# Optimization experiments

Hardware: AMD Instinct MI355X
Metric: run time of the kernel (lower is better)

The kernel has to match this reference:

```python
import jax, jax.numpy as jnp
import numpy as np

BETA = 0.5  # exp-sum normalization exponent (not a true softmax)


def setup_inputs() -> dict:
    key = jax.random.key(0)
    ks = jax.random.split(key, 12)
    b, h = 1024, 200
    item_num, region_num, user_num = 50000, 1000, 10000
    d, hid = 128, 128  # embed_size == hidden_size (required by the bmm reshape)
    std = 0.01
    return {
        "history": jax.random.randint(ks[0], (1, b, h), 0, item_num),
        "target": jax.random.randint(ks[1], (1, b), 0, item_num),
        "history_region": jax.random.randint(ks[2], (1, b, h), 0, region_num),
        "target_region": jax.random.randint(ks[3], (1, b), 0, region_num),
        "history_visit_rate": jax.random.uniform(ks[4], (1, h), dtype=jnp.float32),
        "dist_mat": jax.random.uniform(ks[5], (b, h), dtype=jnp.float32),
        "uid": 7,
        "embed_target": std * jax.random.normal(ks[6], (item_num, d // 2), dtype=jnp.float32),
        "embed_region": std * jax.random.normal(ks[7], (region_num, d // 2), dtype=jnp.float32),
        "embed_dist": std * jax.random.normal(ks[8], (user_num, region_num), dtype=jnp.float32),
        "Wq": jax.random.normal(ks[9], (hid, d), dtype=jnp.float32) * (1.0 / np.sqrt(d)),
        "Wk": jax.random.normal(ks[10], (hid, d), dtype=jnp.float32) * (1.0 / np.sqrt(d)),
        "Wv": jax.random.normal(ks[11], (d, d), dtype=jnp.float32) * (1.0 / np.sqrt(d)),
    }


def reference(history, target, history_region, target_region, history_visit_rate,
              dist_mat, uid, embed_target, embed_region, embed_dist, Wq, Wk, Wv):
    h_idx = history[0]            # [b, h]
    tgt = target[0]               # [b]
    hr = history_region[0]        # [b, h]
    tr = target_region[0]         # [b]
    hv = history_visit_rate[0]    # [h]
    b, hlen = h_idx.shape

    # embedding gathers + concat (target half | region half)
    hist_emb = jnp.concatenate([embed_target[h_idx], embed_region[hr]], axis=-1)  # [b,h,d]
    tgt_emb = jnp.concatenate([embed_target[tgt], embed_region[tr]], axis=-1)     # [b,d]
    hd = embed_dist[uid][hr]      # [b, h]
    td = embed_dist[uid][tr]      # [b]
    d = tgt_emb.shape[1]

    # QKV projections (torch Linear: y = x @ W.T)
    q = tgt_emb @ Wq.T            # [b, d]  (hidden == d)
    k = hist_emb @ Wk.T           # [b, h, d]
    v = hist_emb @ Wv.T           # [b, h, d]

    # faithful to original: key reshaped (NOT transposed) to [b, d, h]
    k_r = k.reshape(b, d, hlen)
    scores = jnp.einsum('bd,bdh->bh', q, k_r) / jnp.sqrt(jnp.float32(d))  # [b,h]

    # exp / beta-normalized attention with equality mask
    mask = (h_idx != tgt[:, None]).astype(scores.dtype)
    exp_A = jnp.exp(scores) * mask                          # [b,h]
    exp_sum = jnp.sum(exp_A, axis=-1) ** BETA               # [b]
    attn = exp_A / exp_sum[:, None]                         # [b,h]

    # geo weights: td @ hd is a vector-matrix product -> [h], broadcast over b
    geo = jnp.exp(-1.0 / (jax.nn.relu(td @ hd) + 1.0) * dist_mat)  # [b,h]

    result1 = v * (attn + geo)[..., None]                   # [b,h,d]
    result2 = hist_emb * jnp.broadcast_to(hv, (b, hlen))[..., None]
    result = result1 + result2                              # [b,h,d]

    pred = jnp.einsum('bhd,bd->b', result, tgt_emb)         # bmm + sum over h
    return jax.nn.sigmoid(pred)
```

## Files before the change

### kernel.cpp

```cpp
#include <hip/hip_runtime.h>

typedef unsigned short USH;
typedef unsigned int   UIN;

static constexpr int Bn = 1024;
static constexpr int Hn = 200;
static constexpr int Dn = 128;
static constexpr int Dh = 64;
static constexpr int NITEM = 50000;
static constexpr int NREG  = 1000;
static constexpr int MT = 64;
static constexpr int AB_A_BLOCKS = (NITEM + MT - 1) / MT;
static constexpr int AB_B_BLOCKS = (NREG  + MT - 1) / MT;
static constexpr int AB_TOT = AB_A_BLOCKS + AB_B_BLOCKS;
static constexpr int QU_BLOCKS = Bn / 4;
static constexpr int WTS = 132;
static constexpr int ETS = 69;
static constexpr int CR  = 50;
static constexpr int AFS = 192;

__device__ __forceinline__ float bf2f(USH u) {
  return __uint_as_float(((UIN)u) << 16);
}
__device__ __forceinline__ float2 pb2f2(UIN p) {
  float2 r;
  r.x = __uint_as_float(p << 16);
  r.y = __uint_as_float(p & 0xffff0000u);
  return r;
}
__device__ __forceinline__ USH f2b(float f) {
  UIN x = __float_as_uint(f);
  return (USH)((x + 0x7fffu + ((x >> 16) & 1u)) >> 16);
}
__device__ __forceinline__ UIN addpk(UIN u, UIN v) {
  float2 a = pb2f2(u), b = pb2f2(v);
  return (UIN)f2b(a.x + b.x) | ((UIN)f2b(a.y + b.y) << 16);
}

__global__ __launch_bounds__(256) void g_kernel(
    const int* __restrict__ hregion, const int* __restrict__ tregion,
    const float* __restrict__ embed_dist, const int* __restrict__ uid,
    float* __restrict__ g) {
  int c = threadIdx.x;
  const float* row = embed_dist + (size_t)uid[0] * NREG;
  float acc = 0.f;
  int ibase = blockIdx.x * 16;
  for (int ii = 0; ii < 16; ii++) {
    int i = ibase + ii;
    float td = row[tregion[i]];
    if (c < Hn) acc += td * row[hregion[(size_t)i * Hn + c]];
  }
  if (c < Hn) atomicAdd(&g[c], acc);
}

__global__ __launch_bounds__(256, 2) void ab_kernel(
    const float* __restrict__ Et, const float* __restrict__ Er,
    const float* __restrict__ Wk, const float* __restrict__ Wq,
    const float* __restrict__ Wv, const int* __restrict__ target,
    const int* __restrict__ tregion,
    USH* __restrict__ Af, USH* __restrict__ Bf,
    float* __restrict__ qvt, float* __restrict__ uvt) {
  __shared__ float wt[64 * WTS];
  __shared__ float et[MT * ETS];
  int blk = blockIdx.x, tid = threadIdx.x;

  if (blk >= AB_TOT) {
    float* te = wt;
    int i0 = (blk - AB_TOT) * 4;
#pragma unroll
    for (int v = 0; v < 2; v++) {
      int idx = v * 256 + tid;
      int ii = idx >> 7, d = idx & 127;
      int it = i0 + ii;
      te[ii * 128 + d] = (d < 64) ? Et[(size_t)target[it] * Dh + d]
                                  : Er[(size_t)tregion[it] * Dh + (d - 64)];
    }
    __syncthreads();
    int j = tid & 127, half = tid >> 7;
    float a0 = 0.f, a1 = 0.f, a2 = 0.f, a3 = 0.f;
    if (half == 0) {
      const float* wr = Wq + (size_t)j * Dn;
#pragma unroll 8
      for (int k = 0; k < 128; k++) {
        float w = wr[k];
        a0 += w * te[k]; a1 += w * te[128 + k];
        a2 += w * te[256 + k]; a3 += w * te[384 + k];
      }
      const float s = 0.088388347648318447f;
      qvt[(size_t)(i0 + 0) * Dn + j] = a0 * s;
      qvt[(size_t)(i0 + 1) * Dn + j] = a1 * s;
      qvt[(size_t)(i0 + 2) * Dn + j] = a2 * s;
      qvt[(size_t)(i0 + 3) * Dn + j] = a3 * s;
    } else {
      int d = j;
#pragma unroll 8
      for (int k = 0; k < 128; k++) {
        float w = Wv[(size_t)k * Dn + d];
        a0 += w * te[k]; a1 += w * te[128 + k];
        a2 += w * te[256 + k]; a3 += w * te[384 + k];
      }
      uvt[(size_t)(i0 + 0) * Dn + d] = a0;
      uvt[(size_t)(i0 + 1) * Dn + d] = a1;
      uvt[(size_t)(i0 + 2) * Dn + d] = a2;
      uvt[(size_t)(i0 + 3) * Dn + d] = a3;
    }
    return;
  }

  const float* E; USH* Out; int nmax, base, koff;
  if (blk < AB_A_BLOCKS) { E = Et; Out = Af; nmax = NITEM; base = blk * MT; koff = 0; }
  else { E = Er; Out = Bf; nmax = NREG; base = (blk - AB_A_BLOCKS) * MT; koff = 64; }

#pragma unroll
  for (int p = 0; p < 8; p++) {
    int idx = p * 256 + tid;
    int row = idx >> 4, c4 = idx & 15;
    float4 w = *reinterpret_cast<const float4*>(Wk + (size_t)row * Dn + koff + c4 * 4);
    wt[(c4 * 4 + 0) * WTS + row] = w.x;
    wt[(c4 * 4 + 1) * WTS + row] = w.y;
    wt[(c4 * 4 + 2) * WTS + row] = w.z;
    wt[(c4 * 4 + 3) * WTS + row] = w.w;
  }
#pragma unroll
  for (int p = 0; p < 4; p++) {
    int idx = p * 256 + tid;
    int m = idx >> 4, c4 = idx & 15;
    int gi = base + m;
    float4 e = make_float4(0.f, 0.f, 0.f, 0.f);
    if (gi < nmax) e = *reinterpret_cast<const float4*>(E + (size_t)gi * Dh + c4 * 4);
    et[m * ETS + c4 * 4 + 0] = e.x;
    et[m * ETS + c4 * 4 + 1] = e.y;
    et[m * ETS + c4 * 4 + 2] = e.z;
    et[m * ETS + c4 * 4 + 3] = e.w;
  }
  __syncthreads();

#pragma unroll
  for (int q = 0; q < 8; q++) {
    int idx = q * 256 + tid;
    int m = idx >> 5, kp = idx & 31;
    int gi = base + m;
    if (gi < nmax) {
      UIN pk = (UIN)f2b(et[m * ETS + 2 * kp]) | ((UIN)f2b(et[m * ETS + 2 * kp + 1]) << 16);
      *reinterpret_cast<UIN*>(Out + (size_t)gi * AFS + 128 + 2 * kp) = pk;
    }
  }

  int jt = tid & 15, it = tid >> 4;
  const float* wb = wt + jt * 8;
  const float* eb = et + (it * 4) * ETS;
  float c[4][8];
#pragma unroll
  for (int ii = 0; ii < 4; ii++)
#pragma unroll
    for (int jj = 0; jj < 8; jj++) c[ii][jj] = 0.f;

#pragma unroll 2
  for (int k = 0; k < 64; k++) {
    float4 w0 = *reinterpret_cast<const float4*>(wb + (size_t)k * WTS);
    float4 w1 = *reinterpret_cast<const float4*>(wb + (size_t)k * WTS + 4);
    float e0 = eb[k], e1 = eb[ETS + k], e2 = eb[2 * ETS + k], e3 = eb[3 * ETS + k];
    c[0][0] += e0 * w0.x; c[0][1] += e0 * w0.y; c[0][2] += e0 * w0.z; c[0][3] += e0 * w0.w;
    c[0][4] += e0 * w1.x; c[0][5] += e0 * w1.y; c[0][6] += e0 * w1.z; c[0][7] += e0 * w1.w;
    c[1][0] += e1 * w0.x; c[1][1] += e1 * w0.y; c[1][2] += e1 * w0.z; c[1][3] += e1 * w0.w;
    c[1][4] += e1 * w1.x; c[1][5] += e1 * w1.y; c[1][6] += e1 * w1.z; c[1][7] += e1 * w1.w;
    c[2][0] += e2 * w0.x; c[2][1] += e2 * w0.y; c[2][2] += e2 * w0.z; c[2][3] += e2 * w0.w;
    c[2][4] += e2 * w1.x; c[2][5] += e2 * w1.y; c[2][6] += e2 * w1.z; c[2][7] += e2 * w1.w;
    c[3][0] += e3 * w0.x; c[3][1] += e3 * w0.y; c[3][2] += e3 * w0.z; c[3][3] += e3 * w0.w;
    c[3][4] += e3 * w1.x; c[3][5] += e3 * w1.y; c[3][6] += e3 * w1.z; c[3][7] += e3 * w1.w;
  }

#pragma unroll
  for (int ii = 0; ii < 4; ii++) {
    int item = base + it * 4 + ii;
    if (item < nmax) {
      uint4 pk;
      pk.x = (UIN)f2b(c[ii][0]) | ((UIN)f2b(c[ii][1]) << 16);
      pk.y = (UIN)f2b(c[ii][2]) | ((UIN)f2b(c[ii][3]) << 16);
      pk.z = (UIN)f2b(c[ii][4]) | ((UIN)f2b(c[ii][5]) << 16);
      pk.w = (UIN)f2b(c[ii][6]) | ((UIN)f2b(c[ii][7]) << 16);
      *reinterpret_cast<uint4*>(Out + (size_t)item * AFS + jt * 8) = pk;
    }
  }
}

__global__ __launch_bounds__(256, 4) void sc_kernel(
    const int* __restrict__ history, const int* __restrict__ target,
    const int* __restrict__ hregion, const int* __restrict__ tregion,
    const float* __restrict__ Et, const float* __restrict__ Er,
    const float* __restrict__ qvt, const float* __restrict__ uvt,
    const USH* __restrict__ Af, const USH* __restrict__ Bf,
    float* __restrict__ psc, float2* __restrict__ s12) {
  __shared__ USH kvs[CR * Dn];
  __shared__ float tgtE[128], uvf[128], qv[32];
  int b = blockIdx.x, i = b >> 2, h = b & 3;
  int tid = threadIdx.x;
  const int* hrow = history + (size_t)i * Hn + CR * h;
  const int* rrow = hregion + (size_t)i * Hn + CR * h;

  if (tid < 128) {
    tgtE[tid] = (tid < 64) ? Et[(size_t)target[i] * Dh + tid]
                           : Er[(size_t)tregion[i] * Dh + (tid - 64)];
  } else {
    uvf[tid - 128] = uvt[(size_t)i * Dn + (tid - 128)];
  }
  if (tid < 32) qv[tid] = qvt[(size_t)i * Dn + 32 * h + tid];

  {
    int rlane = tid & 15, rgrp = tid >> 4;
#pragma unroll
    for (int p = 0; p < 4; p++) {
      int t = p * 16 + rgrp;
      if (t < CR) {
        int ia = hrow[t], ib = rrow[t];
        uint4 av = *reinterpret_cast<const uint4*>(Af + (size_t)ia * AFS + rlane * 8);
        uint4 bv = *reinterpret_cast<const uint4*>(Bf + (size_t)ib * AFS + rlane * 8);
        uint4 pk;
        pk.x = addpk(av.x, bv.x); pk.y = addpk(av.y, bv.y);
        pk.z = addpk(av.z, bv.z); pk.w = addpk(av.w, bv.w);
        *reinterpret_cast<uint4*>(&kvs[t * Dn + rlane * 8]) = pk;
      }
    }
  }
  __syncthreads();

  {
    int l8 = tid & 7, r8 = tid >> 3;
#pragma unroll
    for (int p = 0; p < 2; p++) {
      int t = p * 32 + r8;
      if (t < CR) {
        int ia = hrow[t], ib = rrow[t];
        uint4 e = *reinterpret_cast<const uint4*>(Af + (size_t)ia * AFS + 128 + l8 * 8);
        uint4 r = *reinterpret_cast<const uint4*>(Bf + (size_t)ib * AFS + 128 + l8 * 8);
        float2 e0 = pb2f2(e.x), e1 = pb2f2(e.y), e2 = pb2f2(e.z), e3 = pb2f2(e.w);
        float2 r0 = pb2f2(r.x), r1 = pb2f2(r.y), r2 = pb2f2(r.z), r3 = pb2f2(r.w);
        const float* u0 = &uvf[l8 * 8];       const float* t0 = &tgtE[l8 * 8];
        const float* u1 = &uvf[64 + l8 * 8];  const float* t1 = &tgtE[64 + l8 * 8];
        float s1a = e0.x * u0[0] + e0.y * u0[1] + e1.x * u0[2] + e1.y * u0[3]
                  + e2.x * u0[4] + e2.y * u0[5] + e3.x * u0[6] + e3.y * u0[7]
                  + r0.x * u1[0] + r0.y * u1[1] + r1.x * u1[2] + r1.y * u1[3]
                  + r2.x * u1[4] + r2.y * u1[5] + r3.x * u1[6] + r3.y * u1[7];
        float s2a = e0.x * t0[0] + e0.y * t0[1] + e1.x * t0[2] + e1.y * t0[3]
                  + e2.x * t0[4] + e2.y * t0[5] + e3.x * t0[6] + e3.y * t0[7]
                  + r0.x * t1[0] + r0.y * t1[1] + r1.x * t1[2] + r1.y * t1[3]
                  + r2.x * t1[4] + r2.y * t1[5] + r3.x * t1[6] + r3.y * t1[7];
        s1a += __shfl_xor(s1a, 1, 64); s2a += __shfl_xor(s2a, 1, 64);
        s1a += __shfl_xor(s1a, 2, 64); s2a += __shfl_xor(s2a, 2, 64);
        s1a += __shfl_xor(s1a, 4, 64); s2a += __shfl_xor(s2a, 4, 64);
        if (l8 == 0) s12[(size_t)i * Hn + CR * h + t] = make_float2(s1a, s2a);
      }
    }
  }

  if (tid < Hn) {
    float acc = 0.f;
    const USH* kp = &kvs[tid];
#pragma unroll
    for (int a = 0; a < 32; a++) acc += qv[a] * bf2f(kp[a * 200]);
    psc[((size_t)i * 4 + h) * Hn + tid] = acc;
  }
}

__global__ __launch_bounds__(256, 8) void ep_kernel(
    const int* __restrict__ history, const int* __restrict__ target,
    const float* __restrict__ hv, const float* __restrict__ dist_mat,
    const float* __restrict__ g, const float* __restrict__ psc,
    const float2* __restrict__ s12, float* __restrict__ out) {
  __shared__ float red[8];
  int i = blockIdx.x, tid = threadIdx.x, lane = tid & 63, wave = tid >> 6;
  int tgt_i = target[i];

  float ea = 0.f; float2 sv = make_float2(0.f, 0.f);
  if (tid < Hn) {
    const float* pp = psc + (size_t)i * 4 * Hn + tid;
    float s = (pp[0] + pp[Hn]) + (pp[2 * Hn] + pp[3 * Hn]);
    sv = s12[(size_t)i * Hn + tid];
    ea = (history[(size_t)i * Hn + tid] != tgt_i) ? __expf(s) : 0.f;
  }
  float wsum = ea;
  for (int off = 32; off > 0; off >>= 1) wsum += __shfl_down(wsum, off, 64);
  if (lane == 0) red[wave] = wsum;
  __syncthreads();
  float esum = red[0] + red[1] + red[2] + red[3];
  float inv = esum > 0.f ? 1.f / sqrtf(esum) : 0.f;

  float part = 0.f;
  if (tid < Hn) {
    float gc = g[tid]; gc = gc > 0.f ? gc : 0.f;
    float dm = dist_mat[(size_t)i * Hn + tid];
    float geo = __expf(-dm / (gc + 1.f));
    part = (ea * inv + geo) * sv.x + hv[tid] * sv.y;
  }
  __syncthreads();
  for (int off = 32; off > 0; off >>= 1) part += __shfl_down(part, off, 64);
  if (lane == 0) red[wave] = part;
  __syncthreads();
  if (tid == 0) {
    float pred = red[0] + red[1] + red[2] + red[3];
    out[i] = 1.f / (1.f + __expf(-pred));
  }
}

extern "C" void kernel_launch(void* const* d_in, const int* in_sizes, int n_in,
                              void* d_out, int out_size, void* d_ws, size_t ws_size,
                              hipStream_t stream) {
  const int*   history = (const int*)d_in[0];
  const int*   target  = (const int*)d_in[1];
  const int*   hregion = (const int*)d_in[2];
  const int*   tregion = (const int*)d_in[3];
  const float* hv      = (const float*)d_in[4];
  const float* dist    = (const float*)d_in[5];
  const int*   uid     = (const int*)d_in[6];
  const float* Et      = (const float*)d_in[7];
  const float* Er      = (const float*)d_in[8];
  const float* Edist   = (const float*)d_in[9];
  const float* Wq      = (const float*)d_in[10];
  const float* Wk      = (const float*)d_in[11];
  const float* Wv      = (const float*)d_in[12];

  char* w = (char*)d_ws;
  float* g   = (float*)w;
  USH*   Af  = (USH*)(w + 1024);
  USH*   Bf  = Af + (size_t)NITEM * AFS;
  float* qvt = (float*)(Bf + (size_t)NREG * AFS);
  float* uvt = qvt + (size_t)Bn * Dn;
  float* psc = uvt + (size_t)Bn * Dn;
  float2* s12 = (float2*)(psc + (size_t)Bn * 4 * Hn);
  float* out = (float*)d_out;

  hipMemsetAsync(g, 0, Hn * sizeof(float), stream);
  g_kernel<<<Bn / 16, 256, 0, stream>>>(hregion, tregion, Edist, uid, g);
  ab_kernel<<<AB_TOT + QU_BLOCKS, 256, 0, stream>>>(Et, Er, Wk, Wq, Wv, target,
                                                    tregion, Af, Bf, qvt, uvt);
  sc_kernel<<<Bn * 4, 256, 0, stream>>>(history, target, hregion, tregion,
                                        Et, Er, qvt, uvt, Af, Bf, psc, s12);
  ep_kernel<<<Bn, 256, 0, stream>>>(history, target, hv, dist, g, psc, s12, out);
}
```

Before: 160.2 us.

## Fold geo-weight kernel into ab_kernel and prefetch s12 gathers before barrier

Removes the separate g_kernel launch and runs its work as extra blocks of ab_kernel, cutting one launch and its gap. In sc_kernel, the gathers for the s12 dot products are issued before the __syncthreads so their global-memory latency overlaps the barrier wait and the staging of kvs. This holds more uint4 values in registers across the barrier, which raises register pressure.

```diff
diff --git a/kernel.cpp b/kernel.cpp
--- a/kernel.cpp
+++ b/kernel.cpp
@@ -14,6 +14,7 @@
 static constexpr int AB_B_BLOCKS = (NREG  + MT - 1) / MT;
 static constexpr int AB_TOT = AB_A_BLOCKS + AB_B_BLOCKS;
 static constexpr int QU_BLOCKS = Bn / 4;
+static constexpr int G_BLOCKS  = Bn / 16;
 static constexpr int WTS = 132;
 static constexpr int ETS = 69;
 static constexpr int CR  = 50;
@@ -37,32 +38,31 @@
   return (UIN)f2b(a.x + b.x) | ((UIN)f2b(a.y + b.y) << 16);
 }
 
-__global__ __launch_bounds__(256) void g_kernel(
-    const int* __restrict__ hregion, const int* __restrict__ tregion,
-    const float* __restrict__ embed_dist, const int* __restrict__ uid,
-    float* __restrict__ g) {
-  int c = threadIdx.x;
-  const float* row = embed_dist + (size_t)uid[0] * NREG;
-  float acc = 0.f;
-  int ibase = blockIdx.x * 16;
-  for (int ii = 0; ii < 16; ii++) {
-    int i = ibase + ii;
-    float td = row[tregion[i]];
-    if (c < Hn) acc += td * row[hregion[(size_t)i * Hn + c]];
-  }
-  if (c < Hn) atomicAdd(&g[c], acc);
-}
-
 __global__ __launch_bounds__(256, 2) void ab_kernel(
     const float* __restrict__ Et, const float* __restrict__ Er,
     const float* __restrict__ Wk, const float* __restrict__ Wq,
     const float* __restrict__ Wv, const int* __restrict__ target,
-    const int* __restrict__ tregion,
+    const int* __restrict__ tregion, const int* __restrict__ hregion,
+    const float* __restrict__ embed_dist, const int* __restrict__ uid,
     USH* __restrict__ Af, USH* __restrict__ Bf,
-    float* __restrict__ qvt, float* __restrict__ uvt) {
+    float* __restrict__ qvt, float* __restrict__ uvt, float* __restrict__ g) {
   __shared__ float wt[64 * WTS];
   __shared__ float et[MT * ETS];
   int blk = blockIdx.x, tid = threadIdx.x;
+
+  if (blk >= AB_TOT + QU_BLOCKS) {
+    int c = tid;
+    const float* row = embed_dist + (size_t)uid[0] * NREG;
+    float acc = 0.f;
+    int ibase = (blk - AB_TOT - QU_BLOCKS) * 16;
+    for (int ii = 0; ii < 16; ii++) {
+      int i = ibase + ii;
+      float td = row[tregion[i]];
+      if (c < Hn) acc += td * row[hregion[(size_t)i * Hn + c]];
+    }
+    if (c < Hn) atomicAdd(&g[c], acc);
+    return;
+  }
 
   if (blk >= AB_TOT) {
     float* te = wt;
@@ -222,35 +222,45 @@
       }
     }
   }
-  __syncthreads();
-
+
+  int l8 = tid & 7, r8 = tid >> 3;
+  int ta = r8, tb = 32 + r8;
+  bool hasb = (tb < CR);
+  uint4 ea, ra, eb2, rb2;
   {
-    int l8 = tid & 7, r8 = tid >> 3;
-#pragma unroll
-    for (int p = 0; p < 2; p++) {
-      int t = p * 32 + r8;
-      if (t < CR) {
-        int ia = hrow[t], ib = rrow[t];
-        uint4 e = *reinterpret_cast<const uint4*>(Af + (size_t)ia * AFS + 128 + l8 * 8);
-        uint4 r = *reinterpret_cast<const uint4*>(Bf + (size_t)ib * AFS + 128 + l8 * 8);
-        float2 e0 = pb2f2(e.x), e1 = pb2f2(e.y), e2 = pb2f2(e.z), e3 = pb2f2(e.w);
-        float2 r0 = pb2f2(r.x), r1 = pb2f2(r.y), r2 = pb2f2(r.z), r3 = pb2f2(r.w);
-        const float* u0 = &uvf[l8 * 8];       const float* t0 = &tgtE[l8 * 8];
-        const float* u1 = &uvf[64 + l8 * 8];  const float* t1 = &tgtE[64 + l8 * 8];
-        float s1a = e0.x * u0[0] + e0.y * u0[1] + e1.x * u0[2] + e1.y * u0[3]
-                  + e2.x * u0[4] + e2.y * u0[5] + e3.x * u0[6] + e3.y * u0[7]
-                  + r0.x * u1[0] + r0.y * u1[1] + r1.x * u1[2] + r1.y * u1[3]
-                  + r2.x * u1[4] + r2.y * u1[5] + r3.x * u1[6] + r3.y * u1[7];
-        float s2a = e0.x * t0[0] + e0.y * t0[1] + e1.x * t0[2] + e1.y * t0[3]
-                  + e2.x * t0[4] + e2.y * t0[5] + e3.x * t0[6] + e3.y * t0[7]
-                  + r0.x * t1[0] + r0.y * t1[1] + r1.x * t1[2] + r1.y * t1[3]
-                  + r2.x * t1[4] + r2.y * t1[5] + r3.x * t1[6] + r3.y * t1[7];
-        s1a += __shfl_xor(s1a, 1, 64); s2a += __shfl_xor(s2a, 1, 64);
-        s1a += __shfl_xor(s1a, 2, 64); s2a += __shfl_xor(s2a, 2, 64);
-        s1a += __shfl_xor(s1a, 4, 64); s2a += __shfl_xor(s2a, 4, 64);
-        if (l8 == 0) s12[(size_t)i * Hn + CR * h + t] = make_float2(s1a, s2a);
-      }
-    }
+    int iaa = hrow[ta], iba = rrow[ta];
+    ea = *reinterpret_cast<const uint4*>(Af + (size_t)iaa * AFS + 128 + l8 * 8);
+    ra = *reinterpret_cast<const uint4*>(Bf + (size_t)iba * AFS + 128 + l8 * 8);
+    if (hasb) {
+      int iab = hrow[tb], ibb = rrow[tb];
+      eb2 = *reinterpret_cast<const uint4*>(Af + (size_t)iab * AFS + 128 + l8 * 8);
+      rb2 = *reinterpret_cast<const uint4*>(Bf + (size_t)ibb * AFS + 128 + l8 * 8);
+    }
+  }
+  __syncthreads();
+
+#pragma unroll
+  for (int pass = 0; pass < 2; pass++) {
+    if (pass == 1 && !hasb) break;
+    uint4 e = (pass == 0) ? ea : eb2;
+    uint4 r = (pass == 0) ? ra : rb2;
+    int t = (pass == 0) ? ta : tb;
+    float2 e0 = pb2f2(e.x), e1 = pb2f2(e.y), e2 = pb2f2(e.z), e3 = pb2f2(e.w);
+    float2 r0 = pb2f2(r.x), r1 = pb2f2(r.y), r2 = pb2f2(r.z), r3 = pb2f2(r.w);
+    const float* u0 = &uvf[l8 * 8];       const float* t0 = &tgtE[l8 * 8];
+    const float* u1 = &uvf[64 + l8 * 8];  const float* t1 = &tgtE[64 + l8 * 8];
+    float s1a = e0.x * u0[0] + e0.y * u0[1] + e1.x * u0[2] + e1.y * u0[3]
+              + e2.x * u0[4] + e2.y * u0[5] + e3.x * u0[6] + e3.y * u0[7]
+              + r0.x * u1[0] + r0.y * u1[1] + r1.x * u1[2] + r1.y * u1[3]
+              + r2.x * u1[4] + r2.y * u1[5] + r3.x * u1[6] + r3.y * u1[7];
+    float s2a = e0.x * t0[0] + e0.y * t0[1] + e1.x * t0[2] + e1.y * t0[3]
+              + e2.x * t0[4] + e2.y * t0[5] + e3.x * t0[6] + e3.y * t0[7]
+              + r0.x * t1[0] + r0.y * t1[1] + r1.x * t1[2] + r1.y * t1[3]
+              + r2.x * t1[4] + r2.y * t1[5] + r3.x * t1[6] + r3.y * t1[7];
+    s1a += __shfl_xor(s1a, 1, 64); s2a += __shfl_xor(s2a, 1, 64);
+    s1a += __shfl_xor(s1a, 2, 64); s2a += __shfl_xor(s2a, 2, 64);
+    s1a += __shfl_xor(s1a, 4, 64); s2a += __shfl_xor(s2a, 4, 64);
+    if (l8 == 0) s12[(size_t)i * Hn + CR * h + t] = make_float2(s1a, s2a);
   }
 
   if (tid < Hn) {
@@ -330,9 +340,9 @@
   float* out = (float*)d_out;
 
   hipMemsetAsync(g, 0, Hn * sizeof(float), stream);
-  g_kernel<<<Bn / 16, 256, 0, stream>>>(hregion, tregion, Edist, uid, g);
-  ab_kernel<<<AB_TOT + QU_BLOCKS, 256, 0, stream>>>(Et, Er, Wk, Wq, Wv, target,
-                                                    tregion, Af, Bf, qvt, uvt);
+  ab_kernel<<<AB_TOT + QU_BLOCKS + G_BLOCKS, 256, 0, stream>>>(
+      Et, Er, Wk, Wq, Wv, target, tregion, hregion, Edist, uid,
+      Af, Bf, qvt, uvt, g);
   sc_kernel<<<Bn * 4, 256, 0, stream>>>(history, target, hregion, tregion,
                                         Et, Er, qvt, uvt, Af, Bf, psc, s12);
   ep_kernel<<<Bn, 256, 0, stream>>>(history, target, hv, dist, g, psc, s12, out);
```

New measurement: 153.9 us. 1.04x faster.
